# Kernel optimization log

Hardware: AMD Instinct MI355X
Metric: run time of the kernel (lower is better)

Reference implementation:

```python
import jax, jax.numpy as jnp
import numpy as np

LN_EPS = 1e-5


def setup_inputs() -> dict:
    key = jax.random.key(0)
    ks = jax.random.split(key, 6)
    B, M, N, D = 16, 128, 128, 128
    NM, H = 16, 512
    xav = float(np.sqrt(2.0 / (D + D)))  # xavier_normal over (in_dim, out_dim) fan
    return {
        "x": jax.random.normal(ks[0], (B, M, N, D), jnp.float32),
        "w1": jax.random.normal(ks[1], (D, D, NM, 2), jnp.float32) * xav,
        "w2": jax.random.normal(ks[2], (D, D, NM, 2), jnp.float32) * xav,
        "ff_w0": jax.random.normal(ks[3], (D, H), jnp.float32) * float(1.0 / np.sqrt(D)),
        "ff_b0": jnp.zeros((H,), jnp.float32),
        "ff_w1": jax.random.normal(ks[4], (H, D), jnp.float32) * float(1.0 / np.sqrt(H)),
        "ff_b1": jnp.zeros((D,), jnp.float32),
        "ln_g": jnp.ones((D,), jnp.float32),
        "ln_b": jnp.zeros((D,), jnp.float32),
    }


def _layer_norm(h, g, b):
    mu = jnp.mean(h, axis=-1, keepdims=True)
    var = jnp.mean(jnp.square(h - mu), axis=-1, keepdims=True)
    return (h - mu) * jax.lax.rsqrt(var + LN_EPS) * g + b


def _forward_fourier(x, w1, w2):
    # x: [B, M, N, I] -> [B, I, M, N]
    xt = jnp.transpose(x, (0, 3, 1, 2))
    B, I, M, N = xt.shape
    nm = w1.shape[2]
    cw1 = w1[..., 0] + 1j * w1[..., 1]  # [I, O, nm]
    cw2 = w2[..., 0] + 1j * w2[..., 1]
    O = cw1.shape[1]

    # Fourier along last axis (y)
    fty = jnp.fft.rfft(xt, axis=-1, norm="ortho")                    # [B,I,M,N//2+1]
    f1 = jnp.einsum("bixy,ioy->boxy", fty[..., :nm], cw1)            # [B,O,M,nm]
    pad_y = jnp.zeros((B, O, M, N // 2 + 1 - nm), dtype=f1.dtype)
    xy = jnp.fft.irfft(jnp.concatenate([f1, pad_y], axis=-1), n=N, axis=-1, norm="ortho")

    # Fourier along second-to-last axis (x)
    ftx = jnp.fft.rfft(xt, axis=-2, norm="ortho")                    # [B,I,M//2+1,N]
    f2 = jnp.einsum("bixy,iox->boxy", ftx[:, :, :nm, :], cw2)        # [B,O,nm,N]
    pad_x = jnp.zeros((B, O, M // 2 + 1 - nm, N), dtype=f2.dtype)
    xx = jnp.fft.irfft(jnp.concatenate([f2, pad_x], axis=-2), n=M, axis=-2, norm="ortho")

    return jnp.transpose(xx + xy, (0, 2, 3, 1))  # [B,M,N,O]


def reference(x, w1, w2, ff_w0, ff_b0, ff_w1, ff_b1, ln_g, ln_b):
    h = _forward_fourier(x, w1, w2)
    # backcast FeedForward: Linear -> ReLU -> Linear -> LayerNorm (dropout=0)
    h1 = jax.nn.relu(jnp.einsum("bmni,ih->bmnh", h, ff_w0) + ff_b0)
    h2 = jnp.einsum("bmnh,ho->bmno", h1, ff_w1) + ff_b1
    return _layer_norm(h2, ln_g, ln_b)
```

## Files before the change

kernel.cpp:

```cpp
#include <hip/hip_runtime.h>


#define LN_EPS 1e-5f
#define NMODES 16
#define FROW 4096
#define HROW 16384

typedef __attribute__((ext_vector_type(8))) short short8;
typedef __attribute__((ext_vector_type(8))) ushort ushort8;
typedef __attribute__((ext_vector_type(4))) short short4v;
typedef __attribute__((ext_vector_type(4))) float f32x4;

__device__ __forceinline__ ushort f2bf(float f) {
    unsigned u = __float_as_uint(f);
    unsigned r = (u + 0x7FFFu + ((u >> 16) & 1u)) >> 16;
    return (ushort)r;
}
__device__ __forceinline__ float bf2f(ushort h) {
    return __uint_as_float(((unsigned)h) << 16);
}

__global__ void k_setup(float* __restrict__ Tc, float* __restrict__ Ts,
                        float* __restrict__ IT) {
    const float invs = 0.08838834764831845f;
    for (int idx = threadIdx.x; idx < NMODES * 128; idx += blockDim.x) {
        int k = idx >> 7, n = idx & 127;
        int p = (k * n) & 127;
        float th = (float)p * (6.283185307179586f / 128.0f);
        float c = cosf(th), s = sinf(th);
        Tc[idx] = c * invs;
        Ts[idx] = -s * invs;
        float ck = (k == 0) ? invs : 2.0f * invs;
        IT[n * 32 + 2 * k]     = ck * c;
        IT[n * 32 + 2 * k + 1] = -ck * s;
    }
}

__global__ void k_wpack(const float* __restrict__ w, ushort* __restrict__ Wph,
                        ushort* __restrict__ Wpl) {
    int idx = blockIdx.x * 256 + threadIdx.x;
    int k  = idx >> 16;
    int op = (idx >> 8) & 255;
    int ip = idx & 255;
    int i = ip & 127, o = op & 127;
    const float* base = w + (((i << 7) | o) * NMODES + k) * 2;
    float re = base[0], im = base[1];
    float v = (ip < 128) ? ((op < 128) ? re : im)
                         : ((op < 128) ? -im : re);
    ushort hi = f2bf(v);
    ushort lo = f2bf(v - bf2f(hi));
    Wph[idx] = hi;
    Wpl[idx] = lo;
}

__global__ __launch_bounds__(256) void k_wcvt(const float* __restrict__ w0,
        const float* __restrict__ w1, ushort* __restrict__ w0t,
        ushort* __restrict__ w1t) {
    int idx = blockIdx.x * 256 + threadIdx.x;
    int h = idx >> 7, k = idx & 127;
    w0t[idx] = f2bf(w0[k * 512 + h]);
    int o = idx >> 9, hh = idx & 511;
    w1t[idx] = f2bf(w1[hh * 128 + o]);
}

__global__ __launch_bounds__(128) void k_fft(const float* __restrict__ x,
        const float* __restrict__ Tc, const float* __restrict__ Ts,
        float* __restrict__ F, int mode) {
    __shared__ float Tc_s[NMODES * 128];
    __shared__ float Ts_s[NMODES * 128];
    for (int e = threadIdx.x; e < NMODES * 128; e += 128) {
        Tc_s[e] = Tc[e];
        Ts_s[e] = Ts[e];
    }
    __syncthreads();
    int row = blockIdx.x;
    int base, ts;
    if (mode == 0) { base = row * HROW; ts = 128; }
    else { base = (row >> 7) * 2097152 + (row & 127) * 128; ts = 16384; }
    int i = threadIdx.x;
    float re[NMODES], im[NMODES];
#pragma unroll
    for (int k = 0; k < NMODES; ++k) { re[k] = 0.f; im[k] = 0.f; }
    for (int tb = 0; tb < 32; ++tb) {
        int t0 = tb * 4;
        float xv0 = x[base + (t0 + 0) * ts + i];
        float xv1 = x[base + (t0 + 1) * ts + i];
        float xv2 = x[base + (t0 + 2) * ts + i];
        float xv3 = x[base + (t0 + 3) * ts + i];
#pragma unroll
        for (int k = 0; k < NMODES; ++k) {
            f32x4 c4 = *(const f32x4*)&Tc_s[k * 128 + t0];
            f32x4 s4 = *(const f32x4*)&Ts_s[k * 128 + t0];
            re[k] += xv0 * c4[0] + xv1 * c4[1] + xv2 * c4[2] + xv3 * c4[3];
            im[k] += xv0 * s4[0] + xv1 * s4[1] + xv2 * s4[2] + xv3 * s4[3];
        }
    }
    float* outp = F + row * FROW;
#pragma unroll
    for (int k = 0; k < NMODES; ++k) {
        outp[k * 256 + i]       = re[k];
        outp[k * 256 + 128 + i] = im[k];
    }
}

__global__ __launch_bounds__(256) void k_mixm(const float* __restrict__ A,
        const ushort* __restrict__ Wph, const ushort* __restrict__ Wpl,
        float* __restrict__ outF) {
    __shared__ ushort Ah[32 * 264];
    __shared__ ushort Al[32 * 264];
    int tid = threadIdx.x;
    int kt = blockIdx.x & 15;
    int bm0 = (blockIdx.x >> 4) * 32;
    {
        int row = tid >> 3, cg = tid & 7;
        const float* arow = A + (bm0 + row) * FROW + kt * 256 + cg * 32;
        ushort* ah = &Ah[row * 264 + cg * 32];
        ushort* al = &Al[row * 264 + cg * 32];
#pragma unroll
        for (int j = 0; j < 8; ++j) {
            f32x4 v = *(const f32x4*)(arow + j * 4);
            short4v h4, l4;
#pragma unroll
            for (int q = 0; q < 4; ++q) {
                ushort h = f2bf(v[q]);
                h4[q] = (short)h;
                l4[q] = (short)f2bf(v[q] - bf2f(h));
            }
            *(short4v*)(ah + j * 4) = h4;
            *(short4v*)(al + j * 4) = l4;
        }
    }
    __syncthreads();
    int lane = tid & 63, wid = tid >> 6;
    int frow = lane & 15, fk8 = (lane >> 4) * 8, fr4 = (lane >> 4) * 4;
    f32x4 acc[2][4];
#pragma unroll
    for (int a = 0; a < 2; ++a)
#pragma unroll
        for (int c = 0; c < 4; ++c) acc[a][c] = {0.f, 0.f, 0.f, 0.f};
    const ushort* wph = Wph + kt * 65536;
    const ushort* wpl = Wpl + kt * 65536;
#pragma unroll
    for (int kk = 0; kk < 8; ++kk) {
        short8 ah0 = *(const short8*)&Ah[(frow)      * 264 + kk * 32 + fk8];
        short8 ah1 = *(const short8*)&Ah[(16 + frow) * 264 + kk * 32 + fk8];
        short8 al0 = *(const short8*)&Al[(frow)      * 264 + kk * 32 + fk8];
        short8 al1 = *(const short8*)&Al[(16 + frow) * 264 + kk * 32 + fk8];
#pragma unroll
        for (int tc = 0; tc < 4; ++tc) {
            int op = wid * 64 + tc * 16 + frow;
            int base = op * 256 + kk * 32 + fk8;
            short8 wh = *(const short8*)&wph[base];
            short8 wl = *(const short8*)&wpl[base];
            acc[0][tc] = __builtin_amdgcn_mfma_f32_16x16x32_bf16(ah0, wh, acc[0][tc], 0, 0, 0);
            acc[0][tc] = __builtin_amdgcn_mfma_f32_16x16x32_bf16(ah0, wl, acc[0][tc], 0, 0, 0);
            acc[0][tc] = __builtin_amdgcn_mfma_f32_16x16x32_bf16(al0, wh, acc[0][tc], 0, 0, 0);
            acc[1][tc] = __builtin_amdgcn_mfma_f32_16x16x32_bf16(ah1, wh, acc[1][tc], 0, 0, 0);
            acc[1][tc] = __builtin_amdgcn_mfma_f32_16x16x32_bf16(ah1, wl, acc[1][tc], 0, 0, 0);
            acc[1][tc] = __builtin_amdgcn_mfma_f32_16x16x32_bf16(al1, wh, acc[1][tc], 0, 0, 0);
        }
    }
#pragma unroll
    for (int tr = 0; tr < 2; ++tr)
#pragma unroll
        for (int tc = 0; tc < 4; ++tc)
#pragma unroll
            for (int r = 0; r < 4; ++r)
                outF[(bm0 + tr * 16 + fr4 + r) * FROW + kt * 256 + wid * 64 + tc * 16 + frow]
                    = acc[tr][tc][r];
}

__global__ __launch_bounds__(256) void k_icdft(const float* __restrict__ f,
        const float* __restrict__ IT, ushort* __restrict__ obf,
        float* __restrict__ h32, const ushort* __restrict__ hyin, int mode) {
    __shared__ float IT_s[128 * 32];
    __shared__ float f_s[32 * 128];
    int row = blockIdx.x;
    for (int e = threadIdx.x; e < 4096; e += 256) {
        IT_s[e] = IT[e];
        f_s[e]  = f[row * FROW + e];
    }
    __syncthreads();
    int o = threadIdx.x & 127, nh = threadIdx.x >> 7;
    for (int nb = 0; nb < 8; ++nb) {
        int n0 = nh * 64 + nb * 8;
        float acc[8];
#pragma unroll
        for (int j = 0; j < 8; ++j) acc[j] = 0.f;
#pragma unroll
        for (int kpb = 0; kpb < 8; ++kpb) {
            int kp0 = kpb * 4;
            float f0 = f_s[kp0 * 128 + o];
            float f1v = f_s[kp0 * 128 + 128 + o];
            float f2v = f_s[kp0 * 128 + 256 + o];
            float f3v = f_s[kp0 * 128 + 384 + o];
#pragma unroll
            for (int j = 0; j < 8; ++j) {
                f32x4 it = *(const f32x4*)&IT_s[(n0 + j) * 32 + kp0];
                acc[j] += f0 * it[0] + f1v * it[1] + f2v * it[2] + f3v * it[3];
            }
        }
        if (mode == 0) {
#pragma unroll
            for (int j = 0; j < 8; ++j)
                obf[row * HROW + (n0 + j) * 128 + o] = f2bf(acc[j]);
        } else if (mode == 1) {
#pragma unroll
            for (int j = 0; j < 8; ++j)
                h32[row * HROW + (n0 + j) * 128 + o] = acc[j];
        } else if (mode == 2) {
#pragma unroll
            for (int j = 0; j < 8; ++j) {
                int ix = (row >> 7) * 2097152 + (row & 127) * 128 + o + (n0 + j) * 16384;
                obf[ix] = f2bf(bf2f(hyin[ix]) + acc[j]);
            }
        } else {
#pragma unroll
            for (int j = 0; j < 8; ++j) {
                int ix = (row >> 7) * 2097152 + (row & 127) * 128 + o + (n0 + j) * 16384;
                obf[ix] = f2bf(h32[ix] + acc[j]);
            }
        }
    }
}

__global__ __launch_bounds__(256) void k_ffn1(const ushort* __restrict__ hin,
        const ushort* __restrict__ w0t, const float* __restrict__ b0,
        ushort* __restrict__ h1o) {
    __shared__ ushort A_l[128 * 136];
    __shared__ ushort B_l[64 * 136];
    int tid = threadIdx.x;
    int ht = blockIdx.x & 7, rt = blockIdx.x >> 3;
    int R0 = rt * 128, H0 = ht * 64;

#pragma unroll
    for (int i = 0; i < 8; ++i) {
        int e = tid + i * 256;
        int row = e >> 4, c16 = e & 15;
        *(ushort8*)&A_l[row * 136 + c16 * 8] =
            *(const ushort8*)(hin + (size_t)(R0 + row) * 128 + c16 * 8);
    }
#pragma unroll
    for (int i = 0; i < 4; ++i) {
        int e = tid + i * 256;
        int row = e >> 4, c16 = e & 15;
        *(ushort8*)&B_l[row * 136 + c16 * 8] =
            *(const ushort8*)(w0t + (H0 + row) * 128 + c16 * 8);
    }
    __syncthreads();

    int lane = tid & 63, wave = tid >> 6;
    int frow = lane & 15, qg = lane >> 4, fk8 = qg * 8, fr4 = qg * 4;
    int r2 = wave >> 1, c2 = wave & 1;

    f32x4 acc[4][2];
#pragma unroll
    for (int a = 0; a < 4; ++a)
#pragma unroll
        for (int c = 0; c < 2; ++c) acc[a][c] = {0.f, 0.f, 0.f, 0.f};

#pragma unroll
    for (int kk = 0; kk < 4; ++kk) {
        short8 af[4], bf[2];
#pragma unroll
        for (int tr = 0; tr < 4; ++tr)
            af[tr] = *(const short8*)&A_l[(r2 * 64 + tr * 16 + frow) * 136 + kk * 32 + fk8];
#pragma unroll
        for (int tc = 0; tc < 2; ++tc)
            bf[tc] = *(const short8*)&B_l[(c2 * 32 + tc * 16 + frow) * 136 + kk * 32 + fk8];
#pragma unroll
        for (int tr = 0; tr < 4; ++tr)
#pragma unroll
            for (int tc = 0; tc < 2; ++tc)
                acc[tr][tc] = __builtin_amdgcn_mfma_f32_16x16x32_bf16(
                    af[tr], bf[tc], acc[tr][tc], 0, 0, 0);
    }

    float b0v[2];
    b0v[0] = b0[H0 + c2 * 32 + frow];
    b0v[1] = b0[H0 + c2 * 32 + 16 + frow];
#pragma unroll
    for (int tr = 0; tr < 4; ++tr)
#pragma unroll
        for (int tc = 0; tc < 2; ++tc)
#pragma unroll
            for (int r = 0; r < 4; ++r) {
                int row = r2 * 64 + tr * 16 + fr4 + r;
                int col = H0 + c2 * 32 + tc * 16 + frow;
                h1o[(size_t)(R0 + row) * 512 + col] =
                    f2bf(fmaxf(acc[tr][tc][r] + b0v[tc], 0.f));
            }
}

__global__ __launch_bounds__(256) void k_ffn2(const ushort* __restrict__ h1,
        const ushort* __restrict__ w1t, const float* __restrict__ b1,
        const float* __restrict__ g, const float* __restrict__ bb,
        float* __restrict__ out) {
    __shared__ ushort A_l[32 * 72];
    __shared__ ushort B_l[128 * 72];
    __shared__ float ps_s[128];
    __shared__ float pq_s[128];
    int tid = threadIdx.x;
    int R0 = blockIdx.x * 32;
    int lane = tid & 63, wave = tid >> 6;
    int frow = lane & 15, qg = lane >> 4, fk8 = qg * 8, fr4 = qg * 4;
    int sAr = tid >> 3, sc8 = tid & 7;

    *(ushort8*)&A_l[sAr * 72 + sc8 * 8] =
        *(const ushort8*)(h1 + (size_t)(R0 + sAr) * 512 + sc8 * 8);
#pragma unroll
    for (int i = 0; i < 4; ++i) {
        int ro = sAr + i * 32;
        *(ushort8*)&B_l[ro * 72 + sc8 * 8] =
            *(const ushort8*)(w1t + ro * 512 + sc8 * 8);
    }
    __syncthreads();

    f32x4 acc[2][2];
#pragma unroll
    for (int a = 0; a < 2; ++a)
#pragma unroll
        for (int c = 0; c < 2; ++c) acc[a][c] = {0.f, 0.f, 0.f, 0.f};

#pragma unroll 1
    for (int kt = 0; kt < 8; ++kt) {
        ushort8 sa, sb0, sb1, sb2, sb3;
        if (kt < 7) {
            int koff = (kt + 1) * 64 + sc8 * 8;
            sa  = *(const ushort8*)(h1 + (size_t)(R0 + sAr) * 512 + koff);
            sb0 = *(const ushort8*)(w1t + (sAr +  0) * 512 + koff);
            sb1 = *(const ushort8*)(w1t + (sAr + 32) * 512 + koff);
            sb2 = *(const ushort8*)(w1t + (sAr + 64) * 512 + koff);
            sb3 = *(const ushort8*)(w1t + (sAr + 96) * 512 + koff);
        }
#pragma unroll
        for (int kk = 0; kk < 2; ++kk) {
            short8 af[2], bf[2];
#pragma unroll
            for (int tr = 0; tr < 2; ++tr)
                af[tr] = *(const short8*)&A_l[(tr * 16 + frow) * 72 + kk * 32 + fk8];
#pragma unroll
            for (int tc = 0; tc < 2; ++tc)
                bf[tc] = *(const short8*)&B_l[(wave * 32 + tc * 16 + frow) * 72 + kk * 32 + fk8];
#pragma unroll
            for (int tr = 0; tr < 2; ++tr)
#pragma unroll
                for (int tc = 0; tc < 2; ++tc)
                    acc[tr][tc] = __builtin_amdgcn_mfma_f32_16x16x32_bf16(
                        af[tr], bf[tc], acc[tr][tc], 0, 0, 0);
        }
        __syncthreads();
        if (kt < 7) {
            *(ushort8*)&A_l[sAr * 72 + sc8 * 8] = sa;
            *(ushort8*)&B_l[(sAr +  0) * 72 + sc8 * 8] = sb0;
            *(ushort8*)&B_l[(sAr + 32) * 72 + sc8 * 8] = sb1;
            *(ushort8*)&B_l[(sAr + 64) * 72 + sc8 * 8] = sb2;
            *(ushort8*)&B_l[(sAr + 96) * 72 + sc8 * 8] = sb3;
            __syncthreads();
        }
    }

    float b1v[2], gv[2], bv[2];
#pragma unroll
    for (int tc = 0; tc < 2; ++tc) {
        int o = wave * 32 + tc * 16 + frow;
        b1v[tc] = b1[o]; gv[tc] = g[o]; bv[tc] = bb[o];
    }
#pragma unroll
    for (int tr = 0; tr < 2; ++tr)
#pragma unroll
        for (int r = 0; r < 4; ++r) {
            float s = 0.f, qq = 0.f;
#pragma unroll
            for (int tc = 0; tc < 2; ++tc) {
                float v = acc[tr][tc][r] + b1v[tc];
                acc[tr][tc][r] = v;
                s += v; qq += v * v;
            }
            s += __shfl_xor(s, 1); qq += __shfl_xor(qq, 1);
            s += __shfl_xor(s, 2); qq += __shfl_xor(qq, 2);
            s += __shfl_xor(s, 4); qq += __shfl_xor(qq, 4);
            s += __shfl_xor(s, 8); qq += __shfl_xor(qq, 8);
            if (frow == 0) {
                int row = tr * 16 + fr4 + r;
                ps_s[wave * 32 + row] = s;
                pq_s[wave * 32 + row] = qq;
            }
        }
    __syncthreads();
#pragma unroll
    for (int tr = 0; tr < 2; ++tr)
#pragma unroll
        for (int r = 0; r < 4; ++r) {
            int row = tr * 16 + fr4 + r;
            float S = ps_s[row] + ps_s[32 + row] + ps_s[64 + row] + ps_s[96 + row];
            float Q = pq_s[row] + pq_s[32 + row] + pq_s[64 + row] + pq_s[96 + row];
            float mu = S * (1.0f / 128.0f);
            float var = Q * (1.0f / 128.0f) - mu * mu;
            float rs = rsqrtf(fmaxf(var, 0.f) + LN_EPS);
            float* orow = &out[(size_t)(R0 + row) * 128 + wave * 32];
            orow[frow]      = (acc[tr][0][r] - mu) * rs * gv[0] + bv[0];
            orow[16 + frow] = (acc[tr][1][r] - mu) * rs * gv[1] + bv[1];
        }
}

extern "C" void kernel_launch(void* const* d_in, const int* in_sizes, int n_in,
                              void* d_out, int out_size, void* d_ws, size_t ws_size,
                              hipStream_t stream) {
    (void)in_sizes; (void)n_in; (void)out_size;
    const float* x   = (const float*)d_in[0];
    const float* w1  = (const float*)d_in[1];
    const float* w2  = (const float*)d_in[2];
    const float* fw0 = (const float*)d_in[3];
    const float* fb0 = (const float*)d_in[4];
    const float* fw1 = (const float*)d_in[5];
    const float* fb1 = (const float*)d_in[6];
    const float* lng = (const float*)d_in[7];
    const float* lnb = (const float*)d_in[8];
    float* out = (float*)d_out;

    char* ws = (char*)d_ws;
    float*  Tc  = (float*)(ws);
    float*  Ts  = (float*)(ws + 8192);
    float*  IT  = (float*)(ws + 16384);
    ushort* Wph = (ushort*)(ws + 32768);
    ushort* Wpl = (ushort*)(ws + 32768 + 2097152);
    ushort* w0t = (ushort*)(ws + 4227072);
    ushort* w1t = (ushort*)(ws + 4358144);
    float*  buf0 = (float*)(ws + 4489216);
    ushort* hy   = (ushort*)(ws + 38043648);
    ushort* hsum = (ushort*)(ws + 105152512);
    const size_t need_two = 172261376ull;
    int two = (ws_size >= need_two) ? 1 : 0;
    ushort* hbfs = hy;

    k_setup<<<1, 256, 0, stream>>>(Tc, Ts, IT);
    k_wcvt <<<256, 256, 0, stream>>>(fw0, fw1, w0t, w1t);

    k_wpack<<<4096, 256, 0, stream>>>(w1, Wph, Wpl);
    k_fft  <<<2048, 128, 0, stream>>>(x, Tc, Ts, buf0, 0);
    k_mixm <<<1024, 256, 0, stream>>>(buf0, Wph, Wpl, buf0);
    if (two) k_icdft<<<2048, 256, 0, stream>>>(buf0, IT, hy, out, hy, 0);
    else     k_icdft<<<2048, 256, 0, stream>>>(buf0, IT, hy, out, hy, 1);

    k_wpack<<<4096, 256, 0, stream>>>(w2, Wph, Wpl);
    k_fft  <<<2048, 128, 0, stream>>>(x, Tc, Ts, buf0, 1);
    k_mixm <<<1024, 256, 0, stream>>>(buf0, Wph, Wpl, buf0);
    if (two) k_icdft<<<2048, 256, 0, stream>>>(buf0, IT, hsum, out, hy, 2);
    else     k_icdft<<<2048, 256, 0, stream>>>(buf0, IT, hbfs, out, hy, 3);

    if (two) {
        for (int c = 0; c < 4; ++c) {
            const size_t off = (size_t)c * 65536 * 128;
            k_ffn1<<<4096, 256, 0, stream>>>(hsum + off, w0t, fb0, hy);
            k_ffn2<<<2048, 256, 0, stream>>>(hy, w1t, fb1, lng, lnb, out + off);
        }
    } else {
        ushort* h1buf = (ushort*)buf0;
        for (int c = 0; c < 8; ++c) {
            const size_t off = (size_t)c * 32768 * 128;
            k_ffn1<<<2048, 256, 0, stream>>>(hbfs + off, w0t, fb0, h1buf);
            k_ffn2<<<1024, 256, 0, stream>>>(h1buf, w1t, fb1, lng, lnb, out + off);
        }
    }
}
```

Baseline: 567.4 us.

## Register-block truncated DFT kernel over four columns per thread with prefetch

The truncated DFT kernel now has each thread handle four adjacent columns using float4 loads and stores. Each warp-group of 32 threads covers one row, so a block does four rows and the grid shrinks fourfold. The loads for the next time block are prefetched into registers while the current one is accumulated. This reuses each shared-memory twiddle read across four columns and widens global memory transactions, at the cost of many more accumulator registers (128 floats) and lower occupancy.

Measured after the change: 552.0 us. 1.03x faster.

```diff
diff --git a/kernel.cpp b/kernel.cpp
--- a/kernel.cpp
+++ b/kernel.cpp
@@ -73,33 +73,55 @@
         Ts_s[e] = Ts[e];
     }
     __syncthreads();
-    int row = blockIdx.x;
-    int base, ts;
-    if (mode == 0) { base = row * HROW; ts = 128; }
-    else { base = (row >> 7) * 2097152 + (row & 127) * 128; ts = 16384; }
-    int i = threadIdx.x;
-    float re[NMODES], im[NMODES];
-#pragma unroll
-    for (int k = 0; k < NMODES; ++k) { re[k] = 0.f; im[k] = 0.f; }
+    int row = blockIdx.x * 4 + (threadIdx.x >> 5);
+    int i0 = (threadIdx.x & 31) * 4;
+    size_t base; int ts;
+    if (mode == 0) { base = (size_t)row * HROW; ts = 128; }
+    else { base = (size_t)(row >> 7) * 2097152 + (size_t)(row & 127) * 128; ts = 16384; }
+
+    f32x4 re[NMODES], im[NMODES];
+#pragma unroll
+    for (int k = 0; k < NMODES; ++k) {
+        re[k] = {0.f, 0.f, 0.f, 0.f};
+        im[k] = {0.f, 0.f, 0.f, 0.f};
+    }
+
+    f32x4 xv[4];
+#pragma unroll
+    for (int j = 0; j < 4; ++j)
+        xv[j] = *(const f32x4*)(x + base + (size_t)j * ts + i0);
+
+#pragma unroll 1
     for (int tb = 0; tb < 32; ++tb) {
         int t0 = tb * 4;
-        float xv0 = x[base + (t0 + 0) * ts + i];
-        float xv1 = x[base + (t0 + 1) * ts + i];
-        float xv2 = x[base + (t0 + 2) * ts + i];
-        float xv3 = x[base + (t0 + 3) * ts + i];
+        f32x4 nx[4];
+        if (tb < 31) {
+#pragma unroll
+            for (int j = 0; j < 4; ++j)
+                nx[j] = *(const f32x4*)(x + base + (size_t)(t0 + 4 + j) * ts + i0);
+        }
 #pragma unroll
         for (int k = 0; k < NMODES; ++k) {
             f32x4 c4 = *(const f32x4*)&Tc_s[k * 128 + t0];
             f32x4 s4 = *(const f32x4*)&Ts_s[k * 128 + t0];
-            re[k] += xv0 * c4[0] + xv1 * c4[1] + xv2 * c4[2] + xv3 * c4[3];
-            im[k] += xv0 * s4[0] + xv1 * s4[1] + xv2 * s4[2] + xv3 * s4[3];
-        }
-    }
-    float* outp = F + row * FROW;
+#pragma unroll
+            for (int q = 0; q < 4; ++q) {
+                re[k][q] += xv[0][q] * c4[0] + xv[1][q] * c4[1]
+                          + xv[2][q] * c4[2] + xv[3][q] * c4[3];
+                im[k][q] += xv[0][q] * s4[0] + xv[1][q] * s4[1]
+                          + xv[2][q] * s4[2] + xv[3][q] * s4[3];
+            }
+        }
+        if (tb < 31) {
+#pragma unroll
+            for (int j = 0; j < 4; ++j) xv[j] = nx[j];
+        }
+    }
+    float* outp = F + (size_t)row * FROW;
 #pragma unroll
     for (int k = 0; k < NMODES; ++k) {
-        outp[k * 256 + i]       = re[k];
-        outp[k * 256 + 128 + i] = im[k];
+        *(f32x4*)(outp + k * 256 + i0)       = re[k];
+        *(f32x4*)(outp + k * 256 + 128 + i0) = im[k];
     }
 }
 
@@ -438,13 +460,13 @@
     k_wcvt <<<256, 256, 0, stream>>>(fw0, fw1, w0t, w1t);
 
     k_wpack<<<4096, 256, 0, stream>>>(w1, Wph, Wpl);
-    k_fft  <<<2048, 128, 0, stream>>>(x, Tc, Ts, buf0, 0);
+    k_fft  <<<512, 128, 0, stream>>>(x, Tc, Ts, buf0, 0);
     k_mixm <<<1024, 256, 0, stream>>>(buf0, Wph, Wpl, buf0);
     if (two) k_icdft<<<2048, 256, 0, stream>>>(buf0, IT, hy, out, hy, 0);
     else     k_icdft<<<2048, 256, 0, stream>>>(buf0, IT, hy, out, hy, 1);
 
     k_wpack<<<4096, 256, 0, stream>>>(w2, Wph, Wpl);
-    k_fft  <<<2048, 128, 0, stream>>>(x, Tc, Ts, buf0, 1);
+    k_fft  <<<512, 128, 0, stream>>>(x, Tc, Ts, buf0, 1);
     k_mixm <<<1024, 256, 0, stream>>>(buf0, Wph, Wpl, buf0);
     if (two) k_icdft<<<2048, 256, 0, stream>>>(buf0, IT, hsum, out, hy, 2);
     else     k_icdft<<<2048, 256, 0, stream>>>(buf0, IT, hbfs, out, hy, 3);
```
